# Optimization experiments

Measured on AMD Instinct MI355X. Metric: run time of the kernel, lower is better.

The kernel has to match this reference:

```python
import jax, jax.numpy as jnp
import numpy as np

N_TRAIN, D, B, N_CLASSES, K = 50000, 64, 128, 10, 16


def setup_inputs() -> dict:
    key = jax.random.key(0)
    k1, k2, k3 = jax.random.split(key, 3)
    train_data = jax.random.normal(k1, (N_TRAIN, D), dtype=jnp.float32)
    # one-hot class labels, as implied by gather -> sum over k -> argmax over classes
    labels = jax.random.randint(k2, (N_TRAIN,), 0, N_CLASSES)
    train_target = jax.nn.one_hot(labels, N_CLASSES, dtype=jnp.float32)
    x_test = jax.random.normal(k3, (B, D), dtype=jnp.float32)
    return {"train_data": train_data, "train_target": train_target,
            "x_test": x_test, "k": K}


def reference(train_data, train_target, x_test, k):
    # L1 (Manhattan) distance: [B, N_train]
    # broadcast: [1, N, D] - [B, 1, D] -> abs -> sum over D
    distance = jnp.sum(jnp.abs(train_data[None, :, :] - x_test[:, None, :]), axis=2)
    # top_k of negative distance == k nearest neighbors
    _, top_k_indices = jax.lax.top_k(-distance, k)          # [B, k]
    top_k_label = train_target[top_k_indices]               # [B, k, C] gather
    sum_up_predictions = jnp.sum(top_k_label, axis=1)       # [B, C] vote counts
    return jnp.argmax(sum_up_predictions, axis=1)           # [B] predicted class
```

## Files before the change

kernel.cpp:

```cpp
#include <hip/hip_runtime.h>
#include <cfloat>
#include <climits>

#define NTRAIN 50000
#define DIM 64
#define BQ 128
#define NCLS 10
#define KSEL 16
#define TB 16
#define GROUPS (BQ / TB)
#define THREADS 512
#define TROWS 64
#define TPAD 68

__global__ __launch_bounds__(THREADS) void knn_partial(
    const float* __restrict__ train, const float* __restrict__ xtest,
    float* __restrict__ cand_d, int* __restrict__ cand_i,
    int nslices, int slice_len)
{
    __shared__ float qs[TB * DIM];
    __shared__ float tile[TROWS * TPAD];

    const int bx   = blockIdx.x;
    const int s    = bx % nslices;
    const int g    = bx / nslices;
    const int tid  = threadIdx.x;
    const int w    = tid >> 6;
    const int lane = tid & 63;

    for (int i = tid; i < TB * DIM; i += THREADS)
        qs[i] = xtest[g * TB * DIM + i];
    __syncthreads();

    const int row0 = s * slice_len;
    const int row1 = min(NTRAIN, row0 + slice_len);

    float d0[KSEL], d1[KSEL];
    int   i0[KSEL], i1[KSEL];
#pragma unroll
    for (int j = 0; j < KSEL; ++j) { d0[j] = FLT_MAX; d1[j] = FLT_MAX; i0[j] = INT_MAX; i1[j] = INT_MAX; }

    const float* q0 = &qs[(2 * w)     * DIM];
    const float* q1 = &qs[(2 * w + 1) * DIM];

    for (int base = row0; base < row1; base += TROWS) {
        const int nrows = min(TROWS, row1 - base);
        const int nf4   = nrows * (DIM / 4);
        for (int f = tid; f < nf4; f += THREADS) {
            const int r = f >> 4, c = f & 15;
            const float4 v = *(const float4*)&train[(size_t)(base + r) * DIM + 4 * c];
            *(float4*)&tile[r * TPAD + 4 * c] = v;
        }
        __syncthreads();

        if (lane < nrows) {
            const float* trow = &tile[lane * TPAD];
            double a0 = 0.0, a1 = 0.0;
#pragma unroll
            for (int d4 = 0; d4 < DIM / 4; ++d4) {
                const float4 t  = *(const float4*)&trow[4 * d4];
                const float4 qa = *(const float4*)&q0[4 * d4];
                const float4 qb = *(const float4*)&q1[4 * d4];
                const float s0 = fabsf(t.x - qa.x) + fabsf(t.y - qa.y) +
                                 fabsf(t.z - qa.z) + fabsf(t.w - qa.w);
                const float s1 = fabsf(t.x - qb.x) + fabsf(t.y - qb.y) +
                                 fabsf(t.z - qb.z) + fabsf(t.w - qb.w);
                a0 += (double)s0;
                a1 += (double)s1;
            }
            const float f0 = (float)a0, f1 = (float)a1;
            const int gi = base + lane;
            if (f0 < d0[KSEL - 1]) {
                d0[KSEL - 1] = f0; i0[KSEL - 1] = gi;
#pragma unroll
                for (int j = KSEL - 1; j > 0; --j)
                    if (d0[j] < d0[j - 1]) {
                        float td = d0[j]; d0[j] = d0[j - 1]; d0[j - 1] = td;
                        int   ti = i0[j]; i0[j] = i0[j - 1]; i0[j - 1] = ti;
                    }
            }
            if (f1 < d1[KSEL - 1]) {
                d1[KSEL - 1] = f1; i1[KSEL - 1] = gi;
#pragma unroll
                for (int j = KSEL - 1; j > 0; --j)
                    if (d1[j] < d1[j - 1]) {
                        float td = d1[j]; d1[j] = d1[j - 1]; d1[j - 1] = td;
                        int   ti = i1[j]; i1[j] = i1[j - 1]; i1[j - 1] = ti;
                    }
            }
        }
        __syncthreads();
    }

#pragma unroll
    for (int j = 0; j < 2; ++j) {
        float hd = j ? d1[0] : d0[0];
        int   hi = j ? i1[0] : i0[0];
        int c = 0;
        float od = 0.0f; int oi = 0;
        for (int r = 0; r < KSEL; ++r) {
            float wd = hd; int wi = hi;
#pragma unroll
            for (int sh = 1; sh < 64; sh <<= 1) {
                const float xd = __shfl_xor(wd, sh);
                const int   xi = __shfl_xor(wi, sh);
                if (xd < wd || (xd == wd && xi < wi)) { wd = xd; wi = xi; }
            }
            if (wi == hi) {
                ++c;
                float nd = FLT_MAX; int ni = INT_MAX;
#pragma unroll
                for (int q = 1; q < KSEL; ++q)
                    if (c == q) { nd = j ? d1[q] : d0[q]; ni = j ? i1[q] : i0[q]; }
                hd = nd; hi = ni;
            }
            if (lane == r) { od = wd; oi = wi; }
        }
        const int tp = g * TB + 2 * w + j;
        if (lane < KSEL) {
            cand_d[((size_t)tp * nslices + s) * KSEL + lane] = od;
            cand_i[((size_t)tp * nslices + s) * KSEL + lane] = oi;
        }
    }
}

__global__ __launch_bounds__(64) void knn_final(
    const float* __restrict__ cand_d, const int* __restrict__ cand_i,
    const float* __restrict__ ttarget, int* __restrict__ out, int nslices)
{
    const int b     = blockIdx.x;
    const int lane  = threadIdx.x;
    const int ncand = nslices * KSEL;

    float ld[KSEL]; int li[KSEL];
#pragma unroll
    for (int j = 0; j < KSEL; ++j) { ld[j] = FLT_MAX; li[j] = INT_MAX; }

    for (int q = lane; q < ncand; q += 64) {
        const float dv = cand_d[(size_t)b * ncand + q];
        const int   iv = cand_i[(size_t)b * ncand + q];
        if (dv < ld[KSEL - 1] || (dv == ld[KSEL - 1] && iv < li[KSEL - 1])) {
            ld[KSEL - 1] = dv; li[KSEL - 1] = iv;
#pragma unroll
            for (int j = KSEL - 1; j > 0; --j)
                if (ld[j] < ld[j - 1] || (ld[j] == ld[j - 1] && li[j] < li[j - 1])) {
                    float td = ld[j]; ld[j] = ld[j - 1]; ld[j - 1] = td;
                    int   ti = li[j]; li[j] = li[j - 1]; li[j - 1] = ti;
                }
        }
    }

    float hd = ld[0]; int hi = li[0]; int c = 0;
    float v = 0.0f;
    for (int r = 0; r < KSEL; ++r) {
        float wd = hd; int wi = hi;
#pragma unroll
        for (int sh = 1; sh < 64; sh <<= 1) {
            const float xd = __shfl_xor(wd, sh);
            const int   xi = __shfl_xor(wi, sh);
            if (xd < wd || (xd == wd && xi < wi)) { wd = xd; wi = xi; }
        }
        if (wi == hi) {
            ++c;
            float nd = FLT_MAX; int ni = INT_MAX;
#pragma unroll
            for (int q = 1; q < KSEL; ++q)
                if (c == q) { nd = ld[q]; ni = li[q]; }
            hd = nd; hi = ni;
        }
        if (lane < NCLS) v += ttarget[(size_t)wi * NCLS + lane];
    }

    float bv = (lane < NCLS) ? v : -1.0f;
    int   bc = lane;
#pragma unroll
    for (int sh = 1; sh < 64; sh <<= 1) {
        const float xv = __shfl_xor(bv, sh);
        const int   xc = __shfl_xor(bc, sh);
        if (xv > bv || (xv == bv && xc < bc)) { bv = xv; bc = xc; }
    }
    if (lane == 0) out[b] = bc;
}

extern "C" void kernel_launch(void* const* d_in, const int* in_sizes, int n_in,
                              void* d_out, int out_size, void* d_ws, size_t ws_size,
                              hipStream_t stream) {
    const float* train   = (const float*)d_in[0];
    const float* ttarget = (const float*)d_in[1];
    const float* xtest   = (const float*)d_in[2];
    int* out = (int*)d_out;

    int nslices = 32;
    while (nslices > 1 && (size_t)BQ * nslices * KSEL * 8 > ws_size) nslices >>= 1;
    const int slice_len = (NTRAIN + nslices - 1) / nslices;

    float* cand_d = (float*)d_ws;
    int*   cand_i = (int*)((char*)d_ws + (size_t)BQ * nslices * KSEL * sizeof(float));

    hipLaunchKernelGGL(knn_partial, dim3(GROUPS * nslices), dim3(THREADS), 0, stream,
                       train, xtest, cand_d, cand_i, nslices, slice_len);
    hipLaunchKernelGGL(knn_final, dim3(BQ), dim3(64), 0, stream,
                       cand_d, cand_i, ttarget, out, nslices);
}
```

Baseline: 115.4 us.

## Replace per-thread top-k scan with sampled threshold filter and register-tiled distances

Computes distances from all queries to the first 1024 training rows to get a per-query 16th-smallest threshold. A register-tiled 64x128 distance kernel then scans all training rows and atomically appends any candidate under that threshold to a per-query buffer, and a final kernel selects the top-16 and votes. This drops the per-thread insertion sorts and double-precision accumulation from the main scan and raises arithmetic reuse through 4x8 register tiles. The buffer capacity is bounded, so it overflows if many candidates fall under the threshold. Float summation order also differs from before, which can change tie outcomes.

Measured after the change: 349.0 us. +202.5%, slower.

```diff
diff --git a/kernel.cpp b/kernel.cpp
--- a/kernel.cpp
+++ b/kernel.cpp
@@ -7,138 +7,102 @@
 #define BQ 128
 #define NCLS 10
 #define KSEL 16
-#define TB 16
-#define GROUPS (BQ / TB)
-#define THREADS 512
-#define TROWS 64
+
+#define SAMPLE 1024
+#define CAPMAX 1536
+#define MARGIN 1e-3f
+
 #define TPAD 68
-
-__global__ __launch_bounds__(THREADS) void knn_partial(
+#define BTHREADS 256
+#define TILE_R 128
+#define TILE_Q 64
+#define NSLICE ((NTRAIN + TILE_R - 1) / TILE_R)
+
+__device__ __forceinline__ void tile_distance(
+    const float* __restrict__ qs, const float* __restrict__ ts,
+    int waveQ, int waveR, int qg, int rg, float acc[4][8])
+{
+#pragma unroll
+    for (int i = 0; i < 4; ++i)
+#pragma unroll
+        for (int j = 0; j < 8; ++j) acc[i][j] = 0.0f;
+
+#pragma unroll 4
+    for (int c = 0; c < 16; ++c) {
+        float4 qv[4], tv[8];
+#pragma unroll
+        for (int i = 0; i < 4; ++i)
+            qv[i] = *(const float4*)&qs[(waveQ + qg + 8 * i) * TPAD + 4 * c];
+#pragma unroll
+        for (int j = 0; j < 8; ++j)
+            tv[j] = *(const float4*)&ts[(waveR + rg + 8 * j) * TPAD + 4 * c];
+#pragma unroll
+        for (int i = 0; i < 4; ++i)
+#pragma unroll
+            for (int j = 0; j < 8; ++j) {
+                const float s01 = fabsf(tv[j].x - qv[i].x) + fabsf(tv[j].y - qv[i].y);
+                const float s23 = fabsf(tv[j].z - qv[i].z) + fabsf(tv[j].w - qv[i].w);
+                acc[i][j] += s01 + s23;
+            }
+    }
+}
+
+__device__ __forceinline__ void stage_tiles(
+    float* qs, float* ts, const float* __restrict__ xtest,
+    const float* __restrict__ train, int q0, int r0, int nr, int tid)
+{
+    for (int f = tid; f < TILE_Q * (DIM / 4); f += BTHREADS) {
+        const int q = f >> 4, c = f & 15;
+        *(float4*)&qs[q * TPAD + 4 * c] =
+            *(const float4*)&xtest[(size_t)(q0 + q) * DIM + 4 * c];
+    }
+    for (int f = tid; f < nr * (DIM / 4); f += BTHREADS) {
+        const int r = f >> 4, c = f & 15;
+        *(float4*)&ts[r * TPAD + 4 * c] =
+            *(const float4*)&train[(size_t)(r0 + r) * DIM + 4 * c];
+    }
+    __syncthreads();
+}
+
+__global__ __launch_bounds__(BTHREADS) void knn_sample(
     const float* __restrict__ train, const float* __restrict__ xtest,
-    float* __restrict__ cand_d, int* __restrict__ cand_i,
-    int nslices, int slice_len)
-{
-    __shared__ float qs[TB * DIM];
-    __shared__ float tile[TROWS * TPAD];
-
-    const int bx   = blockIdx.x;
-    const int s    = bx % nslices;
-    const int g    = bx / nslices;
-    const int tid  = threadIdx.x;
-    const int w    = tid >> 6;
-    const int lane = tid & 63;
-
-    for (int i = tid; i < TB * DIM; i += THREADS)
-        qs[i] = xtest[g * TB * DIM + i];
-    __syncthreads();
-
-    const int row0 = s * slice_len;
-    const int row1 = min(NTRAIN, row0 + slice_len);
-
-    float d0[KSEL], d1[KSEL];
-    int   i0[KSEL], i1[KSEL];
-#pragma unroll
-    for (int j = 0; j < KSEL; ++j) { d0[j] = FLT_MAX; d1[j] = FLT_MAX; i0[j] = INT_MAX; i1[j] = INT_MAX; }
-
-    const float* q0 = &qs[(2 * w)     * DIM];
-    const float* q1 = &qs[(2 * w + 1) * DIM];
-
-    for (int base = row0; base < row1; base += TROWS) {
-        const int nrows = min(TROWS, row1 - base);
-        const int nf4   = nrows * (DIM / 4);
-        for (int f = tid; f < nf4; f += THREADS) {
-            const int r = f >> 4, c = f & 15;
-            const float4 v = *(const float4*)&train[(size_t)(base + r) * DIM + 4 * c];
-            *(float4*)&tile[r * TPAD + 4 * c] = v;
-        }
-        __syncthreads();
-
-        if (lane < nrows) {
-            const float* trow = &tile[lane * TPAD];
-            double a0 = 0.0, a1 = 0.0;
-#pragma unroll
-            for (int d4 = 0; d4 < DIM / 4; ++d4) {
-                const float4 t  = *(const float4*)&trow[4 * d4];
-                const float4 qa = *(const float4*)&q0[4 * d4];
-                const float4 qb = *(const float4*)&q1[4 * d4];
-                const float s0 = fabsf(t.x - qa.x) + fabsf(t.y - qa.y) +
-                                 fabsf(t.z - qa.z) + fabsf(t.w - qa.w);
-                const float s1 = fabsf(t.x - qb.x) + fabsf(t.y - qb.y) +
-                                 fabsf(t.z - qb.z) + fabsf(t.w - qb.w);
-                a0 += (double)s0;
-                a1 += (double)s1;
-            }
-            const float f0 = (float)a0, f1 = (float)a1;
-            const int gi = base + lane;
-            if (f0 < d0[KSEL - 1]) {
-                d0[KSEL - 1] = f0; i0[KSEL - 1] = gi;
-#pragma unroll
-                for (int j = KSEL - 1; j > 0; --j)
-                    if (d0[j] < d0[j - 1]) {
-                        float td = d0[j]; d0[j] = d0[j - 1]; d0[j - 1] = td;
-                        int   ti = i0[j]; i0[j] = i0[j - 1]; i0[j - 1] = ti;
-                    }
-            }
-            if (f1 < d1[KSEL - 1]) {
-                d1[KSEL - 1] = f1; i1[KSEL - 1] = gi;
-#pragma unroll
-                for (int j = KSEL - 1; j > 0; --j)
-                    if (d1[j] < d1[j - 1]) {
-                        float td = d1[j]; d1[j] = d1[j - 1]; d1[j - 1] = td;
-                        int   ti = i1[j]; i1[j] = i1[j - 1]; i1[j - 1] = ti;
-                    }
-            }
-        }
-        __syncthreads();
-    }
-
-#pragma unroll
-    for (int j = 0; j < 2; ++j) {
-        float hd = j ? d1[0] : d0[0];
-        int   hi = j ? i1[0] : i0[0];
-        int c = 0;
-        float od = 0.0f; int oi = 0;
-        for (int r = 0; r < KSEL; ++r) {
-            float wd = hd; int wi = hi;
-#pragma unroll
-            for (int sh = 1; sh < 64; sh <<= 1) {
-                const float xd = __shfl_xor(wd, sh);
-                const int   xi = __shfl_xor(wi, sh);
-                if (xd < wd || (xd == wd && xi < wi)) { wd = xd; wi = xi; }
-            }
-            if (wi == hi) {
-                ++c;
-                float nd = FLT_MAX; int ni = INT_MAX;
-#pragma unroll
-                for (int q = 1; q < KSEL; ++q)
-                    if (c == q) { nd = j ? d1[q] : d0[q]; ni = j ? i1[q] : i0[q]; }
-                hd = nd; hi = ni;
-            }
-            if (lane == r) { od = wd; oi = wi; }
-        }
-        const int tp = g * TB + 2 * w + j;
-        if (lane < KSEL) {
-            cand_d[((size_t)tp * nslices + s) * KSEL + lane] = od;
-            cand_i[((size_t)tp * nslices + s) * KSEL + lane] = oi;
-        }
-    }
-}
-
-__global__ __launch_bounds__(64) void knn_final(
-    const float* __restrict__ cand_d, const int* __restrict__ cand_i,
-    const float* __restrict__ ttarget, int* __restrict__ out, int nslices)
-{
-    const int b     = blockIdx.x;
-    const int lane  = threadIdx.x;
-    const int ncand = nslices * KSEL;
-
+    float* __restrict__ samp)
+{
+    __shared__ float qs[TILE_Q * TPAD];
+    __shared__ float ts[TILE_R * TPAD];
+    const int tid = threadIdx.x, w = tid >> 6, lane = tid & 63;
+    const int qg = lane >> 3, rg = lane & 7;
+    const int waveQ = (w >> 1) * 32, waveR = (w & 1) * 64;
+    const int q0 = blockIdx.y * TILE_Q, r0 = blockIdx.x * TILE_R;
+
+    stage_tiles(qs, ts, xtest, train, q0, r0, TILE_R, tid);
+
+    float acc[4][8];
+    tile_distance(qs, ts, waveQ, waveR, qg, rg, acc);
+
+#pragma unroll
+    for (int i = 0; i < 4; ++i) {
+        const int q = q0 + waveQ + qg + 8 * i;
+#pragma unroll
+        for (int j = 0; j < 8; ++j) {
+            const int r = r0 + waveR + rg + 8 * j;
+            samp[(size_t)q * SAMPLE + r] = acc[i][j];
+        }
+    }
+}
+
+__global__ __launch_bounds__(64) void knn_tau(
+    const float* __restrict__ samp, float* __restrict__ tau, int* __restrict__ cnt)
+{
+    const int b = blockIdx.x, lane = threadIdx.x;
     float ld[KSEL]; int li[KSEL];
 #pragma unroll
     for (int j = 0; j < KSEL; ++j) { ld[j] = FLT_MAX; li[j] = INT_MAX; }
 
-    for (int q = lane; q < ncand; q += 64) {
-        const float dv = cand_d[(size_t)b * ncand + q];
-        const int   iv = cand_i[(size_t)b * ncand + q];
+#pragma unroll
+    for (int k = 0; k < SAMPLE / 64; ++k) {
+        const int   iv = lane + 64 * k;
+        const float dv = samp[(size_t)b * SAMPLE + iv];
         if (dv < ld[KSEL - 1] || (dv == ld[KSEL - 1] && iv < li[KSEL - 1])) {
             ld[KSEL - 1] = dv; li[KSEL - 1] = iv;
 #pragma unroll
@@ -150,6 +114,93 @@
         }
     }
 
+    float hd = ld[0]; int hi = li[0]; int c = 0; float last = 0.0f;
+    for (int r = 0; r < KSEL; ++r) {
+        float wd = hd; int wi = hi;
+#pragma unroll
+        for (int sh = 1; sh < 64; sh <<= 1) {
+            const float xd = __shfl_xor(wd, sh);
+            const int   xi = __shfl_xor(wi, sh);
+            if (xd < wd || (xd == wd && xi < wi)) { wd = xd; wi = xi; }
+        }
+        if (wi == hi) {
+            ++c;
+            float nd = FLT_MAX; int ni = INT_MAX;
+#pragma unroll
+            for (int q = 1; q < KSEL; ++q)
+                if (c == q) { nd = ld[q]; ni = li[q]; }
+            hd = nd; hi = ni;
+        }
+        last = wd;
+    }
+    if (lane == 0) { tau[b] = last + MARGIN; cnt[b] = 0; }
+}
+
+__global__ __launch_bounds__(BTHREADS, 3) void knn_scan(
+    const float* __restrict__ train, const float* __restrict__ xtest,
+    const float* __restrict__ tau, int* __restrict__ cnt,
+    float* __restrict__ cand_d, int* __restrict__ cand_i, int cap)
+{
+    __shared__ float qs[TILE_Q * TPAD];
+    __shared__ float ts[TILE_R * TPAD];
+    const int tid = threadIdx.x, w = tid >> 6, lane = tid & 63;
+    const int qg = lane >> 3, rg = lane & 7;
+    const int waveQ = (w >> 1) * 32, waveR = (w & 1) * 64;
+    const int q0 = blockIdx.y * TILE_Q, r0 = blockIdx.x * TILE_R;
+    const int nr = min(TILE_R, NTRAIN - r0);
+
+    stage_tiles(qs, ts, xtest, train, q0, r0, nr, tid);
+
+    float acc[4][8];
+    tile_distance(qs, ts, waveQ, waveR, qg, rg, acc);
+
+    float tv[4];
+#pragma unroll
+    for (int i = 0; i < 4; ++i) tv[i] = tau[q0 + waveQ + qg + 8 * i];
+
+#pragma unroll
+    for (int i = 0; i < 4; ++i) {
+        const int q = q0 + waveQ + qg + 8 * i;
+#pragma unroll
+        for (int j = 0; j < 8; ++j) {
+            const int r = r0 + waveR + rg + 8 * j;
+            if (r < NTRAIN && acc[i][j] <= tv[i]) {
+                const int pos = atomicAdd(&cnt[q], 1);
+                if (pos < cap) {
+                    cand_d[(size_t)q * cap + pos] = acc[i][j];
+                    cand_i[(size_t)q * cap + pos] = r;
+                }
+            }
+        }
+    }
+}
+
+__global__ __launch_bounds__(64) void knn_final(
+    const float* __restrict__ cand_d, const int* __restrict__ cand_i,
+    const int* __restrict__ cnt, const float* __restrict__ ttarget,
+    int* __restrict__ out, int cap)
+{
+    const int b = blockIdx.x, lane = threadIdx.x;
+    const int m = min(cnt[b], cap);
+
+    float ld[KSEL]; int li[KSEL];
+#pragma unroll
+    for (int j = 0; j < KSEL; ++j) { ld[j] = FLT_MAX; li[j] = INT_MAX; }
+
+    for (int q = lane; q < m; q += 64) {
+        const float dv = cand_d[(size_t)b * cap + q];
+        const int   iv = cand_i[(size_t)b * cap + q];
+        if (dv < ld[KSEL - 1] || (dv == ld[KSEL - 1] && iv < li[KSEL - 1])) {
+            ld[KSEL - 1] = dv; li[KSEL - 1] = iv;
+#pragma unroll
+            for (int j = KSEL - 1; j > 0; --j)
+                if (ld[j] < ld[j - 1] || (ld[j] == ld[j - 1] && li[j] < li[j - 1])) {
+                    float td = ld[j]; ld[j] = ld[j - 1]; ld[j - 1] = td;
+                    int   ti = li[j]; li[j] = li[j - 1]; li[j - 1] = ti;
+                }
+        }
+    }
+
     float hd = ld[0]; int hi = li[0]; int c = 0;
     float v = 0.0f;
     for (int r = 0; r < KSEL; ++r) {
@@ -168,7 +219,8 @@
                 if (c == q) { nd = ld[q]; ni = li[q]; }
             hd = nd; hi = ni;
         }
-        if (lane < NCLS) v += ttarget[(size_t)wi * NCLS + lane];
+        if (lane < NCLS && wi >= 0 && wi < NTRAIN)
+            v += ttarget[(size_t)wi * NCLS + lane];
     }
 
     float bv = (lane < NCLS) ? v : -1.0f;
@@ -190,15 +242,25 @@
     const float* xtest   = (const float*)d_in[2];
     int* out = (int*)d_out;
 
-    int nslices = 32;
-    while (nslices > 1 && (size_t)BQ * nslices * KSEL * 8 > ws_size) nslices >>= 1;
-    const int slice_len = (NTRAIN + nslices - 1) / nslices;
-
-    float* cand_d = (float*)d_ws;
-    int*   cand_i = (int*)((char*)d_ws + (size_t)BQ * nslices * KSEL * sizeof(float));
-
-    hipLaunchKernelGGL(knn_partial, dim3(GROUPS * nslices), dim3(THREADS), 0, stream,
-                       train, xtest, cand_d, cand_i, nslices, slice_len);
+    char* ws = (char*)d_ws;
+    float* samp = (float*)ws;
+    float* tau  = (float*)(ws + 524288);
+    int*   cnt  = (int*)(ws + 524800);
+    char*  cand = ws + 525312;
+
+    size_t rem = (ws_size > 525312) ? ws_size - 525312 : 0;
+    size_t cap_s = rem / ((size_t)BQ * 8);
+    int cap = (cap_s > (size_t)CAPMAX) ? CAPMAX : (int)cap_s;
+    if (cap < 64) cap = 64;
+
+    float* cand_d = (float*)cand;
+    int*   cand_i = (int*)(cand + (size_t)BQ * cap * sizeof(float));
+
+    hipLaunchKernelGGL(knn_sample, dim3(SAMPLE / TILE_R, 2), dim3(BTHREADS), 0, stream,
+                       train, xtest, samp);
+    hipLaunchKernelGGL(knn_tau, dim3(BQ), dim3(64), 0, stream, samp, tau, cnt);
+    hipLaunchKernelGGL(knn_scan, dim3(NSLICE, 2), dim3(BTHREADS), 0, stream,
+                       train, xtest, tau, cnt, cand_d, cand_i, cap);
     hipLaunchKernelGGL(knn_final, dim3(BQ), dim3(64), 0, stream,
-                       cand_d, cand_i, ttarget, out, nslices);
-}
+                       cand_d, cand_i, cnt, ttarget, out, cap);
+}
```

## Register-prefetch train tiles, keep queries in registers, double rows per tile

Applied to the files above, without the earlier changes.

Query vectors now live in registers instead of shared memory. The next train tile is prefetched into registers while the current tile is computed, so global load latency overlaps with the distance math. Tile rows double to 128, so each thread computes four distances per tile, giving more ILP and fewer barriers. The cost is much higher register pressure (two 64-float query copies, the prefetch buffers and the top-k arrays), which may lower occupancy or cause spills.

Measured after the change: 283.4 us. 2.46x slower.

```diff
diff --git a/kernel.cpp b/kernel.cpp
--- a/kernel.cpp
+++ b/kernel.cpp
@@ -10,7 +10,7 @@
 #define TB 16
 #define GROUPS (BQ / TB)
 #define THREADS 512
-#define TROWS 64
+#define TROWS 128
 #define TPAD 68
 
 __global__ __launch_bounds__(THREADS) void knn_partial(
@@ -18,7 +18,6 @@
     float* __restrict__ cand_d, int* __restrict__ cand_i,
     int nslices, int slice_len)
 {
-    __shared__ float qs[TB * DIM];
     __shared__ float tile[TROWS * TPAD];
 
     const int bx   = blockIdx.x;
@@ -28,50 +27,79 @@
     const int w    = tid >> 6;
     const int lane = tid & 63;
 
-    for (int i = tid; i < TB * DIM; i += THREADS)
-        qs[i] = xtest[g * TB * DIM + i];
-    __syncthreads();
-
     const int row0 = s * slice_len;
     const int row1 = min(NTRAIN, row0 + slice_len);
 
+    float4 qa[DIM / 4], qb[DIM / 4];
+    {
+        const float* q0p = &xtest[(size_t)(g * TB + 2 * w) * DIM];
+        const float* q1p = q0p + DIM;
+#pragma unroll
+        for (int c = 0; c < DIM / 4; ++c) {
+            qa[c] = *(const float4*)&q0p[4 * c];
+            qb[c] = *(const float4*)&q1p[4 * c];
+        }
+    }
+
     float d0[KSEL], d1[KSEL];
     int   i0[KSEL], i1[KSEL];
 #pragma unroll
     for (int j = 0; j < KSEL; ++j) { d0[j] = FLT_MAX; d1[j] = FLT_MAX; i0[j] = INT_MAX; i1[j] = INT_MAX; }
 
-    const float* q0 = &qs[(2 * w)     * DIM];
-    const float* q1 = &qs[(2 * w + 1) * DIM];
+    const int pr = tid >> 4, pc = tid & 15;
+    float4 pf[4];
+    {
+        const int nr = min(TROWS, row1 - row0);
+#pragma unroll
+        for (int k = 0; k < 4; ++k) {
+            const int r = pr + 32 * k;
+            if (r < nr) pf[k] = *(const float4*)&train[(size_t)(row0 + r) * DIM + 4 * pc];
+        }
+    }
 
     for (int base = row0; base < row1; base += TROWS) {
-        const int nrows = min(TROWS, row1 - base);
-        const int nf4   = nrows * (DIM / 4);
-        for (int f = tid; f < nf4; f += THREADS) {
-            const int r = f >> 4, c = f & 15;
-            const float4 v = *(const float4*)&train[(size_t)(base + r) * DIM + 4 * c];
-            *(float4*)&tile[r * TPAD + 4 * c] = v;
-        }
+        const int nr = min(TROWS, row1 - base);
         __syncthreads();
-
-        if (lane < nrows) {
-            const float* trow = &tile[lane * TPAD];
-            double a0 = 0.0, a1 = 0.0;
-#pragma unroll
-            for (int d4 = 0; d4 < DIM / 4; ++d4) {
-                const float4 t  = *(const float4*)&trow[4 * d4];
-                const float4 qa = *(const float4*)&q0[4 * d4];
-                const float4 qb = *(const float4*)&q1[4 * d4];
-                const float s0 = fabsf(t.x - qa.x) + fabsf(t.y - qa.y) +
-                                 fabsf(t.z - qa.z) + fabsf(t.w - qa.w);
-                const float s1 = fabsf(t.x - qb.x) + fabsf(t.y - qb.y) +
-                                 fabsf(t.z - qb.z) + fabsf(t.w - qb.w);
-                a0 += (double)s0;
-                a1 += (double)s1;
-            }
-            const float f0 = (float)a0, f1 = (float)a1;
-            const int gi = base + lane;
-            if (f0 < d0[KSEL - 1]) {
-                d0[KSEL - 1] = f0; i0[KSEL - 1] = gi;
+#pragma unroll
+        for (int k = 0; k < 4; ++k) {
+            const int r = pr + 32 * k;
+            if (r < nr) *(float4*)&tile[r * TPAD + 4 * pc] = pf[k];
+        }
+        __syncthreads();
+
+        const int nbase = base + TROWS;
+        if (nbase < row1) {
+            const int nnr = min(TROWS, row1 - nbase);
+#pragma unroll
+            for (int k = 0; k < 4; ++k) {
+                const int r = pr + 32 * k;
+                if (r < nnr) pf[k] = *(const float4*)&train[(size_t)(nbase + r) * DIM + 4 * pc];
+            }
+        }
+
+        double a0a = 0.0, a0b = 0.0, a1a = 0.0, a1b = 0.0;
+        const float* tr0 = &tile[lane * TPAD];
+        const float* tr1 = &tile[(lane + 64) * TPAD];
+#pragma unroll
+        for (int c = 0; c < DIM / 4; ++c) {
+            const float4 t0 = *(const float4*)&tr0[4 * c];
+            const float4 t1 = *(const float4*)&tr1[4 * c];
+            const float s0a = fabsf(t0.x - qa[c].x) + fabsf(t0.y - qa[c].y) +
+                              fabsf(t0.z - qa[c].z) + fabsf(t0.w - qa[c].w);
+            const float s0b = fabsf(t0.x - qb[c].x) + fabsf(t0.y - qb[c].y) +
+                              fabsf(t0.z - qb[c].z) + fabsf(t0.w - qb[c].w);
+            const float s1a = fabsf(t1.x - qa[c].x) + fabsf(t1.y - qa[c].y) +
+                              fabsf(t1.z - qa[c].z) + fabsf(t1.w - qa[c].w);
+            const float s1b = fabsf(t1.x - qb[c].x) + fabsf(t1.y - qb[c].y) +
+                              fabsf(t1.z - qb[c].z) + fabsf(t1.w - qb[c].w);
+            a0a += (double)s0a; a0b += (double)s0b;
+            a1a += (double)s1a; a1b += (double)s1b;
+        }
+
+        {
+            const float f = (float)a0a; const int gi = base + lane;
+            if (lane < nr && f < d0[KSEL - 1]) {
+                d0[KSEL - 1] = f; i0[KSEL - 1] = gi;
 #pragma unroll
                 for (int j = KSEL - 1; j > 0; --j)
                     if (d0[j] < d0[j - 1]) {
@@ -79,8 +107,11 @@
                         int   ti = i0[j]; i0[j] = i0[j - 1]; i0[j - 1] = ti;
                     }
             }
-            if (f1 < d1[KSEL - 1]) {
-                d1[KSEL - 1] = f1; i1[KSEL - 1] = gi;
+        }
+        {
+            const float f = (float)a0b; const int gi = base + lane;
+            if (lane < nr && f < d1[KSEL - 1]) {
+                d1[KSEL - 1] = f; i1[KSEL - 1] = gi;
 #pragma unroll
                 for (int j = KSEL - 1; j > 0; --j)
                     if (d1[j] < d1[j - 1]) {
@@ -89,7 +120,30 @@
                     }
             }
         }
-        __syncthreads();
+        {
+            const float f = (float)a1a; const int gi = base + 64 + lane;
+            if (lane + 64 < nr && f < d0[KSEL - 1]) {
+                d0[KSEL - 1] = f; i0[KSEL - 1] = gi;
+#pragma unroll
+                for (int j = KSEL - 1; j > 0; --j)
+                    if (d0[j] < d0[j - 1]) {
+                        float td = d0[j]; d0[j] = d0[j - 1]; d0[j - 1] = td;
+                        int   ti = i0[j]; i0[j] = i0[j - 1]; i0[j - 1] = ti;
+                    }
+            }
+        }
+        {
+            const float f = (float)a1b; const int gi = base + 64 + lane;
+            if (lane + 64 < nr && f < d1[KSEL - 1]) {
+                d1[KSEL - 1] = f; i1[KSEL - 1] = gi;
+#pragma unroll
+                for (int j = KSEL - 1; j > 0; --j)
+                    if (d1[j] < d1[j - 1]) {
+                        float td = d1[j]; d1[j] = d1[j - 1]; d1[j - 1] = td;
+                        int   ti = i1[j]; i1[j] = i1[j - 1]; i1[j - 1] = ti;
+                    }
+            }
+        }
     }
 
 #pragma unroll
```

## Map queries to lanes with register-held queries and broadcast train row loads

Applied to the files above, without the earlier changes.

Restructures the distance scan so that each lane owns one query, held entirely in registers, and each wave streams whole training rows. Every lane reads the same row address, so the load becomes a broadcast and the shared-memory tile and its barriers go away. Accumulation moves from double to float. Per-wave top-k lists are merged in shared memory by one wave, with more stripes and a candidate count passed to the final kernel. The risks are high register pressure from 64 query floats plus the top-k arrays, and a serial merge done by a single wave.

After: 279.8 us. 2.43x slower.

```diff
diff --git a/kernel.cpp b/kernel.cpp
--- a/kernel.cpp
+++ b/kernel.cpp
@@ -7,138 +7,110 @@
 #define BQ 128
 #define NCLS 10
 #define KSEL 16
-#define TB 16
-#define GROUPS (BQ / TB)
-#define THREADS 512
-#define TROWS 64
-#define TPAD 68
+#define WPB 8
+#define SCAN_THREADS (WPB * 64)
 
-__global__ __launch_bounds__(THREADS) void knn_partial(
+__global__ __launch_bounds__(SCAN_THREADS, 2) void knn_scan(
     const float* __restrict__ train, const float* __restrict__ xtest,
     float* __restrict__ cand_d, int* __restrict__ cand_i,
-    int nslices, int slice_len)
+    int stripes, int stripe_len)
 {
-    __shared__ float qs[TB * DIM];
-    __shared__ float tile[TROWS * TPAD];
+    __shared__ float sdl[WPB][64][KSEL];
+    __shared__ int   sil[WPB][64][KSEL];
 
-    const int bx   = blockIdx.x;
-    const int s    = bx % nslices;
-    const int g    = bx / nslices;
-    const int tid  = threadIdx.x;
-    const int w    = tid >> 6;
-    const int lane = tid & 63;
+    const int bx     = blockIdx.x;
+    const int half   = bx & 1;
+    const int stripe = bx >> 1;
+    const int tid    = threadIdx.x;
+    const int lane   = tid & 63;
+    const int w      = __builtin_amdgcn_readfirstlane(tid >> 6);
 
-    for (int i = tid; i < TB * DIM; i += THREADS)
-        qs[i] = xtest[g * TB * DIM + i];
-    __syncthreads();
+    const int r0 = stripe * stripe_len;
+    const int r1 = min(NTRAIN, r0 + stripe_len);
 
-    const int row0 = s * slice_len;
-    const int row1 = min(NTRAIN, row0 + slice_len);
+    const int q = half * 64 + lane;
+    float qreg[DIM];
+    {
+        const float* qp = xtest + (size_t)q * DIM;
+#pragma unroll
+        for (int c = 0; c < DIM / 4; ++c) {
+            const float4 v = *(const float4*)(qp + 4 * c);
+            qreg[4 * c + 0] = v.x; qreg[4 * c + 1] = v.y;
+            qreg[4 * c + 2] = v.z; qreg[4 * c + 3] = v.w;
+        }
+    }
 
-    float d0[KSEL], d1[KSEL];
-    int   i0[KSEL], i1[KSEL];
+    float dk[KSEL]; int ik[KSEL];
 #pragma unroll
-    for (int j = 0; j < KSEL; ++j) { d0[j] = FLT_MAX; d1[j] = FLT_MAX; i0[j] = INT_MAX; i1[j] = INT_MAX; }
+    for (int j = 0; j < KSEL; ++j) { dk[j] = FLT_MAX; ik[j] = INT_MAX; }
 
-    const float* q0 = &qs[(2 * w)     * DIM];
-    const float* q1 = &qs[(2 * w + 1) * DIM];
-
-    for (int base = row0; base < row1; base += TROWS) {
-        const int nrows = min(TROWS, row1 - base);
-        const int nf4   = nrows * (DIM / 4);
-        for (int f = tid; f < nf4; f += THREADS) {
-            const int r = f >> 4, c = f & 15;
-            const float4 v = *(const float4*)&train[(size_t)(base + r) * DIM + 4 * c];
-            *(float4*)&tile[r * TPAD + 4 * c] = v;
+    for (int r = r0 + w; r < r1; r += WPB) {
+        const float* rp = train + (size_t)r * DIM;
+        float a[4] = {0.f, 0.f, 0.f, 0.f};
+#pragma unroll
+        for (int c = 0; c < DIM / 4; ++c) {
+            const float4 t = *(const float4*)(rp + 4 * c);
+            const float s = fabsf(t.x - qreg[4 * c + 0]) + fabsf(t.y - qreg[4 * c + 1]) +
+                            fabsf(t.z - qreg[4 * c + 2]) + fabsf(t.w - qreg[4 * c + 3]);
+            a[c & 3] += s;
         }
-        __syncthreads();
-
-        if (lane < nrows) {
-            const float* trow = &tile[lane * TPAD];
-            double a0 = 0.0, a1 = 0.0;
+        const float d = (a[0] + a[1]) + (a[2] + a[3]);
+        if (d < dk[KSEL - 1]) {
+            dk[KSEL - 1] = d; ik[KSEL - 1] = r;
 #pragma unroll
-            for (int d4 = 0; d4 < DIM / 4; ++d4) {
-                const float4 t  = *(const float4*)&trow[4 * d4];
-                const float4 qa = *(const float4*)&q0[4 * d4];
-                const float4 qb = *(const float4*)&q1[4 * d4];
-                const float s0 = fabsf(t.x - qa.x) + fabsf(t.y - qa.y) +
-                                 fabsf(t.z - qa.z) + fabsf(t.w - qa.w);
-                const float s1 = fabsf(t.x - qb.x) + fabsf(t.y - qb.y) +
-                                 fabsf(t.z - qb.z) + fabsf(t.w - qb.w);
-                a0 += (double)s0;
-                a1 += (double)s1;
-            }
-            const float f0 = (float)a0, f1 = (float)a1;
-            const int gi = base + lane;
-            if (f0 < d0[KSEL - 1]) {
-                d0[KSEL - 1] = f0; i0[KSEL - 1] = gi;
-#pragma unroll
-                for (int j = KSEL - 1; j > 0; --j)
-                    if (d0[j] < d0[j - 1]) {
-                        float td = d0[j]; d0[j] = d0[j - 1]; d0[j - 1] = td;
-                        int   ti = i0[j]; i0[j] = i0[j - 1]; i0[j - 1] = ti;
-                    }
-            }
-            if (f1 < d1[KSEL - 1]) {
-                d1[KSEL - 1] = f1; i1[KSEL - 1] = gi;
-#pragma unroll
-                for (int j = KSEL - 1; j > 0; --j)
-                    if (d1[j] < d1[j - 1]) {
-                        float td = d1[j]; d1[j] = d1[j - 1]; d1[j - 1] = td;
-                        int   ti = i1[j]; i1[j] = i1[j - 1]; i1[j - 1] = ti;
-                    }
-            }
+            for (int j = KSEL - 1; j > 0; --j)
+                if (dk[j] < dk[j - 1]) {
+                    float td = dk[j]; dk[j] = dk[j - 1]; dk[j - 1] = td;
+                    int   ti = ik[j]; ik[j] = ik[j - 1]; ik[j - 1] = ti;
+                }
         }
-        __syncthreads();
     }
 
 #pragma unroll
-    for (int j = 0; j < 2; ++j) {
-        float hd = j ? d1[0] : d0[0];
-        int   hi = j ? i1[0] : i0[0];
-        int c = 0;
-        float od = 0.0f; int oi = 0;
-        for (int r = 0; r < KSEL; ++r) {
-            float wd = hd; int wi = hi;
+    for (int j = 0; j < KSEL; ++j) { sdl[w][lane][j] = dk[j]; sil[w][lane][j] = ik[j]; }
+    __syncthreads();
+
+    if (w == 0) {
+        float md[KSEL]; int mi[KSEL];
 #pragma unroll
-            for (int sh = 1; sh < 64; sh <<= 1) {
-                const float xd = __shfl_xor(wd, sh);
-                const int   xi = __shfl_xor(wi, sh);
-                if (xd < wd || (xd == wd && xi < wi)) { wd = xd; wi = xi; }
+        for (int j = 0; j < KSEL; ++j) { md[j] = FLT_MAX; mi[j] = INT_MAX; }
+        for (int v = 0; v < WPB; ++v)
+            for (int j = 0; j < KSEL; ++j) {
+                const float f  = sdl[v][lane][j];
+                const int   fi = sil[v][lane][j];
+                if (f < md[KSEL - 1] || (f == md[KSEL - 1] && fi < mi[KSEL - 1])) {
+                    md[KSEL - 1] = f; mi[KSEL - 1] = fi;
+#pragma unroll
+                    for (int t = KSEL - 1; t > 0; --t)
+                        if (md[t] < md[t - 1] || (md[t] == md[t - 1] && mi[t] < mi[t - 1])) {
+                            float td = md[t]; md[t] = md[t - 1]; md[t - 1] = td;
+                            int   ti = mi[t]; mi[t] = mi[t - 1]; mi[t - 1] = ti;
+                        }
+                }
             }
-            if (wi == hi) {
-                ++c;
-                float nd = FLT_MAX; int ni = INT_MAX;
+        const int ncand = stripes * KSEL;
 #pragma unroll
-                for (int q = 1; q < KSEL; ++q)
-                    if (c == q) { nd = j ? d1[q] : d0[q]; ni = j ? i1[q] : i0[q]; }
-                hd = nd; hi = ni;
-            }
-            if (lane == r) { od = wd; oi = wi; }
-        }
-        const int tp = g * TB + 2 * w + j;
-        if (lane < KSEL) {
-            cand_d[((size_t)tp * nslices + s) * KSEL + lane] = od;
-            cand_i[((size_t)tp * nslices + s) * KSEL + lane] = oi;
+        for (int j = 0; j < KSEL; ++j) {
+            cand_d[(size_t)q * ncand + stripe * KSEL + j] = md[j];
+            cand_i[(size_t)q * ncand + stripe * KSEL + j] = mi[j];
         }
     }
 }
 
 __global__ __launch_bounds__(64) void knn_final(
     const float* __restrict__ cand_d, const int* __restrict__ cand_i,
-    const float* __restrict__ ttarget, int* __restrict__ out, int nslices)
+    const float* __restrict__ ttarget, int* __restrict__ out, int ncand)
 {
-    const int b     = blockIdx.x;
-    const int lane  = threadIdx.x;
-    const int ncand = nslices * KSEL;
+    const int b    = blockIdx.x;
+    const int lane = threadIdx.x;
 
     float ld[KSEL]; int li[KSEL];
 #pragma unroll
     for (int j = 0; j < KSEL; ++j) { ld[j] = FLT_MAX; li[j] = INT_MAX; }
 
-    for (int q = lane; q < ncand; q += 64) {
-        const float dv = cand_d[(size_t)b * ncand + q];
-        const int   iv = cand_i[(size_t)b * ncand + q];
+    for (int c = lane; c < ncand; c += 64) {
+        const float dv = cand_d[(size_t)b * ncand + c];
+        const int   iv = cand_i[(size_t)b * ncand + c];
         if (dv < ld[KSEL - 1] || (dv == ld[KSEL - 1] && iv < li[KSEL - 1])) {
             ld[KSEL - 1] = dv; li[KSEL - 1] = iv;
 #pragma unroll
@@ -164,8 +136,8 @@
             ++c;
             float nd = FLT_MAX; int ni = INT_MAX;
 #pragma unroll
-            for (int q = 1; q < KSEL; ++q)
-                if (c == q) { nd = ld[q]; ni = li[q]; }
+            for (int t = 1; t < KSEL; ++t)
+                if (c == t) { nd = ld[t]; ni = li[t]; }
             hd = nd; hi = ni;
         }
         if (lane < NCLS) v += ttarget[(size_t)wi * NCLS + lane];
@@ -190,15 +162,16 @@
     const float* xtest   = (const float*)d_in[2];
     int* out = (int*)d_out;
 
-    int nslices = 32;
-    while (nslices > 1 && (size_t)BQ * nslices * KSEL * 8 > ws_size) nslices >>= 1;
-    const int slice_len = (NTRAIN + nslices - 1) / nslices;
+    int stripes = 128;
+    while (stripes > 16 && (size_t)BQ * stripes * KSEL * 8 > ws_size) stripes >>= 1;
+    const int stripe_len = (NTRAIN + stripes - 1) / stripes;
+    const int ncand = stripes * KSEL;
 
     float* cand_d = (float*)d_ws;
-    int*   cand_i = (int*)((char*)d_ws + (size_t)BQ * nslices * KSEL * sizeof(float));
+    int*   cand_i = (int*)((char*)d_ws + (size_t)BQ * ncand * sizeof(float));
 
-    hipLaunchKernelGGL(knn_partial, dim3(GROUPS * nslices), dim3(THREADS), 0, stream,
-                       train, xtest, cand_d, cand_i, nslices, slice_len);
+    hipLaunchKernelGGL(knn_scan, dim3(2 * stripes), dim3(SCAN_THREADS), 0, stream,
+                       train, xtest, cand_d, cand_i, stripes, stripe_len);
     hipLaunchKernelGGL(knn_final, dim3(BQ), dim3(64), 0, stream,
-                       cand_d, cand_i, ttarget, out, nslices);
+                       cand_d, cand_i, ttarget, out, ncand);
 }
```
